# Optimization experiments

Measured on AMD Instinct MI355X. Metric: run time of the kernel, lower is better.

Reference implementation:

```python
import jax, jax.numpy as jnp
import numpy as np

A, B, SDIM, HID, NH = 16, 65536, 64, 32, 4
ADIM = HID // NH  # attend_dim = 8


def setup_inputs() -> dict:
    key = jax.random.key(0)
    ks = jax.random.split(key, 9)
    sc = 0.1
    return {
        "states": jax.random.normal(ks[0], (A, B, SDIM), dtype=jnp.float32),
        "Ws": jax.random.normal(ks[1], (SDIM, HID), dtype=jnp.float32) * sc,
        "bs": jax.random.normal(ks[2], (HID,), dtype=jnp.float32) * sc,
        "Wk": jax.random.normal(ks[3], (NH, HID, ADIM), dtype=jnp.float32) * sc,
        "Wq": jax.random.normal(ks[4], (NH, HID, ADIM), dtype=jnp.float32) * sc,
        "Wv": jax.random.normal(ks[5], (NH, HID, ADIM), dtype=jnp.float32) * sc,
        "bv": jax.random.normal(ks[6], (NH, ADIM), dtype=jnp.float32) * sc,
        "Wc": jax.random.normal(ks[7], (2 * HID, HID), dtype=jnp.float32) * sc,
        "bc": jax.random.normal(ks[8], (HID,), dtype=jnp.float32) * sc,
    }


def reference(states, Ws, bs, Wk, Wq, Wv, bv, Wc, bc):
    lrelu = lambda x: jax.nn.leaky_relu(x, 0.01)  # torch LeakyReLU default slope
    # shared state encoder over all agents: [A,B,HID]
    enc = lrelu(jnp.einsum('abs,sh->abh', states, Ws) + bs)
    s_enc = enc[0]                                   # agent-0 selector source [B,HID]
    oth = enc[1:]                                    # other agents [A-1,B,HID]
    keys = jnp.einsum('abh,nhd->nabd', oth, Wk)      # [NH,A-1,B,d]
    vals = lrelu(jnp.einsum('abh,nhd->nabd', oth, Wv) + bv[:, None, None, :])
    sel = jnp.einsum('bh,nhd->nbd', s_enc, Wq)       # [NH,B,d]
    scale = 1.0 / np.sqrt(np.float32(ADIM))
    logits = jnp.einsum('nbd,nabd->nba', sel, keys) * scale  # [NH,B,A-1]
    w = jax.nn.softmax(logits, axis=-1)
    other = jnp.einsum('nba,nabd->nbd', w, vals)     # [NH,B,d]
    other_flat = jnp.transpose(other, (1, 0, 2)).reshape(s_enc.shape[0], NH * ADIM)
    critic_in = jnp.concatenate([s_enc, other_flat], axis=1)  # [B, 2*HID]
    all_q = critic_in @ Wc + bc                      # [B, HID]
    return all_q
```

## Files before the change

kernel.cpp:

```cpp
#include <hip/hip_runtime.h>

#define NB 65536
#define SCALE 0.35355339059327373f

typedef float  f32x4  __attribute__((ext_vector_type(4)));
typedef float  f32x8  __attribute__((ext_vector_type(8)));
typedef short  s16x8  __attribute__((ext_vector_type(8)));
typedef __bf16 bf16x8 __attribute__((ext_vector_type(8)));

static __device__ __forceinline__ s16x8 cvt8(f32x8 f) {
    return __builtin_bit_cast(s16x8, __builtin_convertvector(f, bf16x8));
}
static __device__ __forceinline__ float lrelu(float x) { return x > 0.f ? x : 0.01f * x; }

#define MFMA(A, B, C) __builtin_amdgcn_mfma_f32_16x16x32_bf16((A), (B), (C), 0, 0, 0)

__global__ __launch_bounds__(256) void gru_attn_mfma(
    const float* __restrict__ states,
    const float* __restrict__ Ws,  const float* __restrict__ bs,
    const float* __restrict__ Wk,  const float* __restrict__ Wq,
    const float* __restrict__ Wv,  const float* __restrict__ bv,
    const float* __restrict__ Wc,  const float* __restrict__ bc,
    float* __restrict__ out)
{
    __shared__ s16x8  wtab[14][64];
    __shared__ float4 cinS[4][256];

    const int tid = threadIdx.x;
    const int l   = tid & 63;
    const int wid = tid >> 6;
    const int g   = l >> 4;
    const int lr  = l & 15;

    for (int f = wid; f < 14; f += 4) {
        f32x8 v;
#pragma unroll
        for (int i = 0; i < 8; ++i) {
            float x;
            if (f < 4)       { const int kc = f >> 1, nh = f & 1;  x = Ws[(kc*32 + g*8 + i)*32 + nh*16 + lr]; }
            else if (f < 6)  { const int hd = (f-4)*16 + lr;       x = Wk[(hd>>3)*256 + (g*8 + i)*8 + (hd&7)]; }
            else if (f < 8)  { const int hd = (f-6)*16 + lr;       x = Wv[(hd>>3)*256 + (g*8 + i)*8 + (hd&7)]; }
            else if (f < 10) { const int hd = (f-8)*16 + lr;       x = Wq[(hd>>3)*256 + (g*8 + i)*8 + (hd&7)]; }
            else             { const int t = f-10, kc = t >> 1, nh = t & 1;
                               x = Wc[(kc*32 + g*8 + i)*32 + nh*16 + lr]; }
            v[i] = x;
        }
        wtab[f][l] = cvt8(v);
    }
    __syncthreads();

    const float bs0 = bs[lr], bs1 = bs[16 + lr];
    const float bv0 = bv[lr], bv1 = bv[16 + lr];

    const int btile = blockIdx.x * 4 + wid;
    const int b0    = btile * 16;

    char* cinb = (char*)cinS[wid];
    const float* sbase = states + (size_t)(b0 + lr) * 64 + g * 8;

    const s16x8 w0 = wtab[0][l], w1 = wtab[1][l], w2 = wtab[2][l], w3 = wtab[3][l];
    const s16x8 w4 = wtab[4][l], w5 = wtab[5][l], w6 = wtab[6][l], w7 = wtab[7][l];

    const f32x4 zf4 = {0.f, 0.f, 0.f, 0.f};
    f32x4 qa0 = zf4, qa1 = zf4;
    f32x4 ot0 = zf4, ot1 = zf4;
    f32x4 ll0 = zf4, ll1 = zf4;
    f32x4 mm0 = {-1e30f, -1e30f, -1e30f, -1e30f};
    f32x4 mm1 = mm0;

    float4 buf0[4], buf1[4];

#define LOADA(BUF, a) { const float* p = sbase + (size_t)(a) * ((size_t)NB * 64); \
    BUF[0] = *(const float4*)(p);      BUF[1] = *(const float4*)(p + 4); \
    BUF[2] = *(const float4*)(p + 32); BUF[3] = *(const float4*)(p + 36); }

#define CVTAB(BUF, AF0, AF1) { \
    f32x8 fA = {BUF[0].x, BUF[0].y, BUF[0].z, BUF[0].w, BUF[1].x, BUF[1].y, BUF[1].z, BUF[1].w}; \
    f32x8 fB = {BUF[2].x, BUF[2].y, BUF[2].z, BUF[2].w, BUF[3].x, BUF[3].y, BUF[3].z, BUF[3].w}; \
    AF0 = cvt8(fA); AF1 = cvt8(fB); }

#define ENCODE(AF0, AF1, E0, E1) \
    f32x4 E0 = {bs0, bs0, bs0, bs0}, E1 = {bs1, bs1, bs1, bs1}; \
    E0 = MFMA(AF0, w0, E0); E0 = MFMA(AF1, w2, E0); \
    E1 = MFMA(AF0, w1, E1); E1 = MFMA(AF1, w3, E1); \
    _Pragma("unroll") for (int r = 0; r < 4; ++r) { E0[r] = lrelu(E0[r]); E1[r] = lrelu(E1[r]); }

#define ATTN(E0, E1) { \
    _Pragma("unroll") for (int r = 0; r < 4; ++r) { const int bb = g*4 + r; \
        *(float*)(cinb + bb*256 + 128 + ((lr*4     ) ^ ((bb&7)<<4))) = E0[r]; \
        *(float*)(cinb + bb*256 + 128 + ((64 + lr*4) ^ ((bb&7)<<4))) = E1[r]; } \
    const float4 r0 = *(const float4*)(cinb + lr*256 + 128 + ((g*32     ) ^ ((lr&7)<<4))); \
    const float4 r1 = *(const float4*)(cinb + lr*256 + 128 + ((g*32 + 16) ^ ((lr&7)<<4))); \
    f32x8 fe = {r0.x, r0.y, r0.z, r0.w, r1.x, r1.y, r1.z, r1.w}; \
    const s16x8 ef = cvt8(fe); \
    f32x4 k0 = MFMA(ef, w4, zf4); \
    f32x4 k1 = MFMA(ef, w5, zf4); \
    f32x4 v0 = {bv0, bv0, bv0, bv0}, v1 = {bv1, bv1, bv1, bv1}; \
    v0 = MFMA(ef, w6, v0); \
    v1 = MFMA(ef, w7, v1); \
    f32x4 p0 = qa0 * k0, p1 = qa1 * k1; \
    _Pragma("unroll") for (int r = 0; r < 4; ++r) { \
        v0[r] = lrelu(v0[r]); v1[r] = lrelu(v1[r]); \
        float s0 = p0[r]; s0 += __shfl_xor(s0, 1); s0 += __shfl_xor(s0, 2); s0 += __shfl_xor(s0, 4); \
        float s1 = p1[r]; s1 += __shfl_xor(s1, 1); s1 += __shfl_xor(s1, 2); s1 += __shfl_xor(s1, 4); \
        const float z0 = s0 * SCALE, z1 = s1 * SCALE; \
        const float n0 = fmaxf(mm0[r], z0), n1 = fmaxf(mm1[r], z1); \
        const float c0 = __expf(mm0[r] - n0), c1 = __expf(mm1[r] - n1); \
        const float p0s = __expf(z0 - n0),  p1s = __expf(z1 - n1); \
        ll0[r] = ll0[r]*c0 + p0s;  ll1[r] = ll1[r]*c1 + p1s; \
        ot0[r] = ot0[r]*c0 + p0s*v0[r];  ot1[r] = ot1[r]*c1 + p1s*v1[r]; \
        mm0[r] = n0;  mm1[r] = n1; \
    } }

    LOADA(buf0, 0)
    LOADA(buf1, 1)

    {
        s16x8 af0, af1; CVTAB(buf0, af0, af1)
        LOADA(buf0, 2)
        ENCODE(af0, af1, e0, e1)
#pragma unroll
        for (int r = 0; r < 4; ++r) { const int bb = g*4 + r;
            *(float*)(cinb + bb*256 + ((lr*4     ) ^ ((bb&7)<<4))) = e0[r];
            *(float*)(cinb + bb*256 + ((64 + lr*4) ^ ((bb&7)<<4))) = e1[r]; }
        const float4 r0 = *(const float4*)(cinb + lr*256 + ((g*32     ) ^ ((lr&7)<<4)));
        const float4 r1 = *(const float4*)(cinb + lr*256 + ((g*32 + 16) ^ ((lr&7)<<4)));
        f32x8 fq = {r0.x, r0.y, r0.z, r0.w, r1.x, r1.y, r1.z, r1.w};
        const s16x8 ef = cvt8(fq);
        qa0 = MFMA(ef, wtab[8][l], zf4);
        qa1 = MFMA(ef, wtab[9][l], zf4);
    }
    {
        s16x8 af0, af1; CVTAB(buf1, af0, af1)
        LOADA(buf1, 3)
        ENCODE(af0, af1, e0, e1)
        ATTN(e0, e1)
    }
#pragma unroll 1
    for (int a = 2; a < 14; a += 2) {
        {
            s16x8 af0, af1; CVTAB(buf0, af0, af1)
            LOADA(buf0, a + 2)
            ENCODE(af0, af1, e0, e1)
            ATTN(e0, e1)
        }
        {
            s16x8 af0, af1; CVTAB(buf1, af0, af1)
            LOADA(buf1, a + 3)
            ENCODE(af0, af1, e0, e1)
            ATTN(e0, e1)
        }
    }
    {
        s16x8 af0, af1; CVTAB(buf0, af0, af1)
        ENCODE(af0, af1, e0, e1)
        ATTN(e0, e1)
    }
    {
        s16x8 af0, af1; CVTAB(buf1, af0, af1)
        ENCODE(af0, af1, e0, e1)
        ATTN(e0, e1)
    }

#pragma unroll
    for (int r = 0; r < 4; ++r) {
        const int bb = g*4 + r;
        const float i0 = 1.0f / ll0[r], i1 = 1.0f / ll1[r];
        *(float*)(cinb + bb*256 + 128 + ((lr*4     ) ^ ((bb&7)<<4))) = ot0[r] * i0;
        *(float*)(cinb + bb*256 + 128 + ((64 + lr*4) ^ ((bb&7)<<4))) = ot1[r] * i1;
    }

    {
        const float bc0 = bc[lr], bc1 = bc[16 + lr];
        const float4 c00 = *(const float4*)(cinb + lr*256 + ((g*32           ) ^ ((lr&7)<<4)));
        const float4 c01 = *(const float4*)(cinb + lr*256 + ((g*32 + 16      ) ^ ((lr&7)<<4)));
        const float4 c10 = *(const float4*)(cinb + lr*256 + 128 + ((g*32     ) ^ ((lr&7)<<4)));
        const float4 c11 = *(const float4*)(cinb + lr*256 + 128 + ((g*32 + 16) ^ ((lr&7)<<4)));
        f32x8 fc0 = {c00.x, c00.y, c00.z, c00.w, c01.x, c01.y, c01.z, c01.w};
        f32x8 fc1 = {c10.x, c10.y, c10.z, c10.w, c11.x, c11.y, c11.z, c11.w};
        const s16x8 cf0 = cvt8(fc0), cf1 = cvt8(fc1);
        f32x4 o0 = {bc0, bc0, bc0, bc0}, o1 = {bc1, bc1, bc1, bc1};
        o0 = MFMA(cf0, wtab[10][l], o0);  o0 = MFMA(cf1, wtab[12][l], o0);
        o1 = MFMA(cf0, wtab[11][l], o1);  o1 = MFMA(cf1, wtab[13][l], o1);
#pragma unroll
        for (int r = 0; r < 4; ++r) {
            const int bb = g*4 + r;
            out[(size_t)(b0 + bb)*32 + lr]      = o0[r];
            out[(size_t)(b0 + bb)*32 + 16 + lr] = o1[r];
        }
    }
}

extern "C" void kernel_launch(void* const* d_in, const int* in_sizes, int n_in,
                              void* d_out, int out_size, void* d_ws, size_t ws_size,
                              hipStream_t stream) {
    const float* states = (const float*)d_in[0];
    const float* Ws     = (const float*)d_in[1];
    const float* bs     = (const float*)d_in[2];
    const float* Wk     = (const float*)d_in[3];
    const float* Wq     = (const float*)d_in[4];
    const float* Wv     = (const float*)d_in[5];
    const float* bv     = (const float*)d_in[6];
    const float* Wc     = (const float*)d_in[7];
    const float* bc     = (const float*)d_in[8];
    float* out          = (float*)d_out;

    gru_attn_mfma<<<dim3(NB / 64), dim3(256), 0, stream>>>(
        states, Ws, bs, Wk, Wq, Wv, bv, Wc, bc, out);
}
```

Baseline: 56.70 us.

## Process two batch tiles per wave and drop softmax max tracking

Each wave now loops over two consecutive 16-row batch tiles, halving the grid, amortizing the weight-table setup and prefetching the next tile's first agent states during the current tail. The online softmax no longer tracks a running max and rescales; it exponentiates the logits directly, with the scale folded into the query. This removes per-agent exp and max work but risks overflow for large logits. The kernel is already close to streaming-bandwidth bound.

After: 51.21 us, median of 3. 9.7% less time.

```diff
diff --git a/kernel.cpp b/kernel.cpp
--- a/kernel.cpp
+++ b/kernel.cpp
@@ -2,6 +2,7 @@
 
 #define NB 65536
 #define SCALE 0.35355339059327373f
+#define AGSTR ((size_t)NB * 64)
 
 typedef float  f32x4  __attribute__((ext_vector_type(4)));
 typedef float  f32x8  __attribute__((ext_vector_type(8)));
@@ -52,27 +53,18 @@
     const float bs0 = bs[lr], bs1 = bs[16 + lr];
     const float bv0 = bv[lr], bv1 = bv[16 + lr];
 
-    const int btile = blockIdx.x * 4 + wid;
-    const int b0    = btile * 16;
-
     char* cinb = (char*)cinS[wid];
-    const float* sbase = states + (size_t)(b0 + lr) * 64 + g * 8;
 
     const s16x8 w0 = wtab[0][l], w1 = wtab[1][l], w2 = wtab[2][l], w3 = wtab[3][l];
     const s16x8 w4 = wtab[4][l], w5 = wtab[5][l], w6 = wtab[6][l], w7 = wtab[7][l];
 
     const f32x4 zf4 = {0.f, 0.f, 0.f, 0.f};
-    f32x4 qa0 = zf4, qa1 = zf4;
-    f32x4 ot0 = zf4, ot1 = zf4;
-    f32x4 ll0 = zf4, ll1 = zf4;
-    f32x4 mm0 = {-1e30f, -1e30f, -1e30f, -1e30f};
-    f32x4 mm1 = mm0;
 
     float4 buf0[4], buf1[4];
 
-#define LOADA(BUF, a) { const float* p = sbase + (size_t)(a) * ((size_t)NB * 64); \
-    BUF[0] = *(const float4*)(p);      BUF[1] = *(const float4*)(p + 4); \
-    BUF[2] = *(const float4*)(p + 32); BUF[3] = *(const float4*)(p + 36); }
+#define LOADP(BUF, p) { \
+    BUF[0] = *(const float4*)(p);      BUF[1] = *(const float4*)((p) + 4); \
+    BUF[2] = *(const float4*)((p) + 32); BUF[3] = *(const float4*)((p) + 36); }
 
 #define CVTAB(BUF, AF0, AF1) { \
     f32x8 fA = {BUF[0].x, BUF[0].y, BUF[0].z, BUF[0].w, BUF[1].x, BUF[1].y, BUF[1].z, BUF[1].w}; \
@@ -103,90 +95,103 @@
         v0[r] = lrelu(v0[r]); v1[r] = lrelu(v1[r]); \
         float s0 = p0[r]; s0 += __shfl_xor(s0, 1); s0 += __shfl_xor(s0, 2); s0 += __shfl_xor(s0, 4); \
         float s1 = p1[r]; s1 += __shfl_xor(s1, 1); s1 += __shfl_xor(s1, 2); s1 += __shfl_xor(s1, 4); \
-        const float z0 = s0 * SCALE, z1 = s1 * SCALE; \
-        const float n0 = fmaxf(mm0[r], z0), n1 = fmaxf(mm1[r], z1); \
-        const float c0 = __expf(mm0[r] - n0), c1 = __expf(mm1[r] - n1); \
-        const float p0s = __expf(z0 - n0),  p1s = __expf(z1 - n1); \
-        ll0[r] = ll0[r]*c0 + p0s;  ll1[r] = ll1[r]*c1 + p1s; \
-        ot0[r] = ot0[r]*c0 + p0s*v0[r];  ot1[r] = ot1[r]*c1 + p1s*v1[r]; \
-        mm0[r] = n0;  mm1[r] = n1; \
+        const float p0s = __expf(s0), p1s = __expf(s1); \
+        ll0[r] += p0s;  ll1[r] += p1s; \
+        ot0[r] += p0s * v0[r];  ot1[r] += p1s * v1[r]; \
     } }
 
-    LOADA(buf0, 0)
-    LOADA(buf1, 1)
-
-    {
-        s16x8 af0, af1; CVTAB(buf0, af0, af1)
-        LOADA(buf0, 2)
-        ENCODE(af0, af1, e0, e1)
-#pragma unroll
-        for (int r = 0; r < 4; ++r) { const int bb = g*4 + r;
-            *(float*)(cinb + bb*256 + ((lr*4     ) ^ ((bb&7)<<4))) = e0[r];
-            *(float*)(cinb + bb*256 + ((64 + lr*4) ^ ((bb&7)<<4))) = e1[r]; }
-        const float4 r0 = *(const float4*)(cinb + lr*256 + ((g*32     ) ^ ((lr&7)<<4)));
-        const float4 r1 = *(const float4*)(cinb + lr*256 + ((g*32 + 16) ^ ((lr&7)<<4)));
-        f32x8 fq = {r0.x, r0.y, r0.z, r0.w, r1.x, r1.y, r1.z, r1.w};
-        const s16x8 ef = cvt8(fq);
-        qa0 = MFMA(ef, wtab[8][l], zf4);
-        qa1 = MFMA(ef, wtab[9][l], zf4);
-    }
-    {
-        s16x8 af0, af1; CVTAB(buf1, af0, af1)
-        LOADA(buf1, 3)
-        ENCODE(af0, af1, e0, e1)
-        ATTN(e0, e1)
-    }
+    const int bbase = blockIdx.x * 128 + wid * 32;
+    const float* sb0 = states + (size_t)(bbase + lr) * 64 + g * 8;
+
+    LOADP(buf0, sb0)
+    LOADP(buf1, sb0 + AGSTR)
+
 #pragma unroll 1
-    for (int a = 2; a < 14; a += 2) {
+    for (int t = 0; t < 2; ++t) {
+        const int b0 = bbase + t * 16;
+        const float* sbase = states + (size_t)(b0 + lr) * 64 + g * 8;
+
+        f32x4 qa0 = zf4, qa1 = zf4;
+        f32x4 ot0 = zf4, ot1 = zf4;
+        f32x4 ll0 = zf4, ll1 = zf4;
+
         {
             s16x8 af0, af1; CVTAB(buf0, af0, af1)
-            LOADA(buf0, a + 2)
+            LOADP(buf0, sbase + 2 * AGSTR)
+            ENCODE(af0, af1, e0, e1)
+#pragma unroll
+            for (int r = 0; r < 4; ++r) { const int bb = g*4 + r;
+                *(float*)(cinb + bb*256 + ((lr*4     ) ^ ((bb&7)<<4))) = e0[r];
+                *(float*)(cinb + bb*256 + ((64 + lr*4) ^ ((bb&7)<<4))) = e1[r]; }
+            const float4 r0 = *(const float4*)(cinb + lr*256 + ((g*32     ) ^ ((lr&7)<<4)));
+            const float4 r1 = *(const float4*)(cinb + lr*256 + ((g*32 + 16) ^ ((lr&7)<<4)));
+            f32x8 fq = {r0.x, r0.y, r0.z, r0.w, r1.x, r1.y, r1.z, r1.w};
+            const s16x8 ef = cvt8(fq);
+            qa0 = MFMA(ef, wtab[8][l], zf4);
+            qa1 = MFMA(ef, wtab[9][l], zf4);
+            qa0 = qa0 * SCALE;
+            qa1 = qa1 * SCALE;
+        }
+        {
+            s16x8 af0, af1; CVTAB(buf1, af0, af1)
+            LOADP(buf1, sbase + 3 * AGSTR)
             ENCODE(af0, af1, e0, e1)
             ATTN(e0, e1)
         }
+#pragma unroll 1
+        for (int a = 2; a < 14; a += 2) {
+            {
+                s16x8 af0, af1; CVTAB(buf0, af0, af1)
+                LOADP(buf0, sbase + (size_t)(a + 2) * AGSTR)
+                ENCODE(af0, af1, e0, e1)
+                ATTN(e0, e1)
+            }
+            {
+                s16x8 af0, af1; CVTAB(buf1, af0, af1)
+                LOADP(buf1, sbase + (size_t)(a + 3) * AGSTR)
+                ENCODE(af0, af1, e0, e1)
+                ATTN(e0, e1)
+            }
+        }
+        {
+            s16x8 af0, af1; CVTAB(buf0, af0, af1)
+            if (t == 0) { LOADP(buf0, sbase + 16 * 64) }
+            ENCODE(af0, af1, e0, e1)
+            ATTN(e0, e1)
+        }
         {
             s16x8 af0, af1; CVTAB(buf1, af0, af1)
-            LOADA(buf1, a + 3)
+            if (t == 0) { LOADP(buf1, sbase + 16 * 64 + AGSTR) }
             ENCODE(af0, af1, e0, e1)
             ATTN(e0, e1)
         }
-    }
-    {
-        s16x8 af0, af1; CVTAB(buf0, af0, af1)
-        ENCODE(af0, af1, e0, e1)
-        ATTN(e0, e1)
-    }
-    {
-        s16x8 af0, af1; CVTAB(buf1, af0, af1)
-        ENCODE(af0, af1, e0, e1)
-        ATTN(e0, e1)
-    }
-
-#pragma unroll
-    for (int r = 0; r < 4; ++r) {
-        const int bb = g*4 + r;
-        const float i0 = 1.0f / ll0[r], i1 = 1.0f / ll1[r];
-        *(float*)(cinb + bb*256 + 128 + ((lr*4     ) ^ ((bb&7)<<4))) = ot0[r] * i0;
-        *(float*)(cinb + bb*256 + 128 + ((64 + lr*4) ^ ((bb&7)<<4))) = ot1[r] * i1;
-    }
-
-    {
-        const float bc0 = bc[lr], bc1 = bc[16 + lr];
-        const float4 c00 = *(const float4*)(cinb + lr*256 + ((g*32           ) ^ ((lr&7)<<4)));
-        const float4 c01 = *(const float4*)(cinb + lr*256 + ((g*32 + 16      ) ^ ((lr&7)<<4)));
-        const float4 c10 = *(const float4*)(cinb + lr*256 + 128 + ((g*32     ) ^ ((lr&7)<<4)));
-        const float4 c11 = *(const float4*)(cinb + lr*256 + 128 + ((g*32 + 16) ^ ((lr&7)<<4)));
-        f32x8 fc0 = {c00.x, c00.y, c00.z, c00.w, c01.x, c01.y, c01.z, c01.w};
-        f32x8 fc1 = {c10.x, c10.y, c10.z, c10.w, c11.x, c11.y, c11.z, c11.w};
-        const s16x8 cf0 = cvt8(fc0), cf1 = cvt8(fc1);
-        f32x4 o0 = {bc0, bc0, bc0, bc0}, o1 = {bc1, bc1, bc1, bc1};
-        o0 = MFMA(cf0, wtab[10][l], o0);  o0 = MFMA(cf1, wtab[12][l], o0);
-        o1 = MFMA(cf0, wtab[11][l], o1);  o1 = MFMA(cf1, wtab[13][l], o1);
+
 #pragma unroll
         for (int r = 0; r < 4; ++r) {
             const int bb = g*4 + r;
-            out[(size_t)(b0 + bb)*32 + lr]      = o0[r];
-            out[(size_t)(b0 + bb)*32 + 16 + lr] = o1[r];
+            const float i0 = 1.0f / ll0[r], i1 = 1.0f / ll1[r];
+            *(float*)(cinb + bb*256 + 128 + ((lr*4     ) ^ ((bb&7)<<4))) = ot0[r] * i0;
+            *(float*)(cinb + bb*256 + 128 + ((64 + lr*4) ^ ((bb&7)<<4))) = ot1[r] * i1;
+        }
+
+        {
+            const float bc0 = bc[lr], bc1 = bc[16 + lr];
+            const float4 c00 = *(const float4*)(cinb + lr*256 + ((g*32           ) ^ ((lr&7)<<4)));
+            const float4 c01 = *(const float4*)(cinb + lr*256 + ((g*32 + 16      ) ^ ((lr&7)<<4)));
+            const float4 c10 = *(const float4*)(cinb + lr*256 + 128 + ((g*32     ) ^ ((lr&7)<<4)));
+            const float4 c11 = *(const float4*)(cinb + lr*256 + 128 + ((g*32 + 16) ^ ((lr&7)<<4)));
+            f32x8 fc0 = {c00.x, c00.y, c00.z, c00.w, c01.x, c01.y, c01.z, c01.w};
+            f32x8 fc1 = {c10.x, c10.y, c10.z, c10.w, c11.x, c11.y, c11.z, c11.w};
+            const s16x8 cf0 = cvt8(fc0), cf1 = cvt8(fc1);
+            f32x4 o0 = {bc0, bc0, bc0, bc0}, o1 = {bc1, bc1, bc1, bc1};
+            o0 = MFMA(cf0, wtab[10][l], o0);  o0 = MFMA(cf1, wtab[12][l], o0);
+            o1 = MFMA(cf0, wtab[11][l], o1);  o1 = MFMA(cf1, wtab[13][l], o1);
+#pragma unroll
+            for (int r = 0; r < 4; ++r) {
+                const int bb = g*4 + r;
+                out[(size_t)(b0 + bb)*32 + lr]      = o0[r];
+                out[(size_t)(b0 + bb)*32 + 16 + lr] = o1[r];
+            }
         }
     }
 }
@@ -205,6 +210,6 @@
     const float* bc     = (const float*)d_in[8];
     float* out          = (float*)d_out;
 
-    gru_attn_mfma<<<dim3(NB / 64), dim3(256), 0, stream>>>(
+    gru_attn_mfma<<<dim3(NB / 128), dim3(256), 0, stream>>>(
         states, Ws, bs, Wk, Wq, Wv, bv, Wc, bc, out);
 }
```
